# Kernel optimization log

Hardware: AMD Instinct MI355X
Metric: run time of the kernel (lower is better)

Reference implementation:

```python
import jax, jax.numpy as jnp
import numpy as np

N_NODES = 100000
N_EDGES = 1600000
IN_DIM, HID, OUT = 6, 64, 32


def _linear_params(key, fan_in, fan_out):
    k1, k2 = jax.random.split(key)
    bound = 1.0 / np.sqrt(fan_in)
    W = jax.random.uniform(k1, (fan_in, fan_out), jnp.float32, -bound, bound)
    b = jax.random.uniform(k2, (fan_out,), jnp.float32, -bound, bound)
    return W, b


def setup_inputs() -> dict:
    key = jax.random.key(0)
    ks = jax.random.split(key, 9)
    x = jax.random.normal(ks[0], (N_NODES, IN_DIM), jnp.float32)
    edge_index = jax.random.randint(ks[1], (2, N_EDGES), 0, N_NODES, jnp.int64)
    edge_attr = jax.random.normal(ks[2], (N_EDGES, 3), jnp.float32)
    W1a, b1a = _linear_params(ks[3], IN_DIM + 3, HID)
    W1b, b1b = _linear_params(ks[4], HID, HID)
    W2a, b2a = _linear_params(ks[5], HID + 3, HID)
    W2b, b2b = _linear_params(ks[6], HID, HID)
    W3a, b3a = _linear_params(ks[7], HID + 3, OUT)
    W3b, b3b = _linear_params(ks[8], OUT, OUT)
    return {
        "x": x, "edge_index": edge_index, "edge_attr": edge_attr,
        "W1a": W1a, "b1a": b1a, "W1b": W1b, "b1b": b1b,
        "W2a": W2a, "b2a": b2a, "W2b": W2b, "b2b": b2b,
        "W3a": W3a, "b3a": b3a, "W3b": W3b, "b3b": b3b,
    }


def _gnn_layer(x, src, dst, edge_attr, Wa, ba, Wb, bb):
    # message: per-edge 2-layer MLP on [x_j, edge_attr]
    msg = jnp.concatenate([x[src], edge_attr], axis=-1)       # [E, in+3]
    h = jax.nn.relu(msg @ Wa + ba) @ Wb + bb                   # [E, out]
    # aggr='mean': scatter-sum into target nodes, divide by in-degree
    s = jax.ops.segment_sum(h, dst, num_segments=N_NODES)     # [N, out]
    cnt = jax.ops.segment_sum(jnp.ones((src.shape[0],), x.dtype), dst,
                              num_segments=N_NODES)
    return s / jnp.maximum(cnt, 1.0)[:, None]


def reference(x, edge_index, edge_attr,
              W1a, b1a, W1b, b1b,
              W2a, b2a, W2b, b2b,
              W3a, b3a, W3b, b3b):
    src, dst = edge_index[0], edge_index[1]   # x_j = x[src], aggregate at dst
    h = _gnn_layer(x, src, dst, edge_attr, W1a, b1a, W1b, b1b)
    h = jax.nn.relu(h)
    h = _gnn_layer(h, src, dst, edge_attr, W2a, b2a, W2b, b2b)
    h = jax.nn.relu(h)
    out = _gnn_layer(h, src, dst, edge_attr, W3a, b3a, W3b, b3b)
    return out
```

## Files before the change

### kernel.cpp

```cpp
#include <hip/hip_runtime.h>
#include <hip/hip_fp16.h>

#define N_NODES 100000
#define N_EDGES 1600000

__global__ __launch_bounds__(256) void degree_kernel(const int* __restrict__ dst,
                                                     int* __restrict__ cnt, int E) {
    const int range = blockIdx.x & 7;
    const int lo = range * (N_NODES / 8);
    const int hi = lo + (N_NODES / 8);
    int i = (blockIdx.x >> 3) * blockDim.x + threadIdx.x;
    const int stride = (gridDim.x >> 3) * blockDim.x;
    for (; i < E; i += stride) {
        const int d = dst[i];
        if (d >= lo && d < hi) atomicAdd(&cnt[d], 1);
    }
}

__global__ __launch_bounds__(256) void inv_kernel(const int* __restrict__ cnt,
                                                  float* __restrict__ inv, int N) {
    int i = blockIdx.x * blockDim.x + threadIdx.x;
    if (i < N) inv[i] = (cnt[i] > 0) ? (1.0f / (float)cnt[i]) : 0.0f;
}

__global__ __launch_bounds__(256) void block_sum_kernel(const int* __restrict__ cnt,
                                                        int* __restrict__ bsum, int N) {
    __shared__ int s[256];
    const int tid = threadIdx.x;
    const int i = blockIdx.x * 256 + tid;
    s[tid] = (i < N) ? cnt[i] : 0;
    __syncthreads();
#pragma unroll
    for (int d = 128; d > 0; d >>= 1) {
        if (tid < d) s[tid] += s[tid + d];
        __syncthreads();
    }
    if (tid == 0) bsum[blockIdx.x] = s[0];
}

__global__ __launch_bounds__(512) void scan_bsum_kernel(int* __restrict__ bsum, int NB) {
    __shared__ int s[512];
    const int tid = threadIdx.x;
    const int v = (tid < NB) ? bsum[tid] : 0;
    s[tid] = v;
    __syncthreads();
    for (int d = 1; d < 512; d <<= 1) {
        const int t = (tid >= d) ? s[tid - d] : 0;
        __syncthreads();
        s[tid] += t;
        __syncthreads();
    }
    if (tid < NB) bsum[tid] = s[tid] - v;
}

__global__ __launch_bounds__(256) void make_cursor_kernel(const int* __restrict__ cnt,
                                                          const int* __restrict__ bsum,
                                                          int* __restrict__ cursor, int N) {
    __shared__ int s[256];
    const int tid = threadIdx.x;
    const int i = blockIdx.x * 256 + tid;
    const int v = (i < N) ? cnt[i] : 0;
    s[tid] = v;
    __syncthreads();
    for (int d = 1; d < 256; d <<= 1) {
        const int t = (tid >= d) ? s[tid - d] : 0;
        __syncthreads();
        s[tid] += t;
        __syncthreads();
    }
    if (i < N) cursor[i] = bsum[blockIdx.x] + s[tid] - v;
}

__global__ __launch_bounds__(256) void scatter_pack_kernel(
    const int* __restrict__ src, const int* __restrict__ dst,
    const float* __restrict__ ea,
    int* __restrict__ cursor, float4* __restrict__ spf, int E) {
    const int range = blockIdx.x & 7;
    const int lo = range * (N_NODES / 8);
    const int hi = lo + (N_NODES / 8);
    int i = (blockIdx.x >> 3) * blockDim.x + threadIdx.x;
    const int stride = (gridDim.x >> 3) * blockDim.x;
    for (; i < E; i += stride) {
        const int d = dst[i];
        if (d >= lo && d < hi) {
            const int pos = atomicAdd(&cursor[d], 1);
            spf[pos] = make_float4(__int_as_float(src[i]),
                                   ea[3 * (size_t)i + 0],
                                   ea[3 * (size_t)i + 1],
                                   ea[3 * (size_t)i + 2]);
        }
    }
}

__global__ __launch_bounds__(256) void node_gemm6h(
    const float* __restrict__ x, const float* __restrict__ W,
    const float* __restrict__ bias, __half* __restrict__ out_, int N) {
    int n = blockIdx.x * blockDim.x + threadIdx.x;
    if (n >= N) return;
    const float* row = x + (size_t)n * 6;
    float v[6];
#pragma unroll
    for (int k = 0; k < 6; ++k) v[k] = row[k];
    __half2* orow = (__half2*)(out_ + (size_t)n * 64);
    for (int g = 0; g < 16; ++g) {
        float a0 = bias[4 * g + 0], a1 = bias[4 * g + 1];
        float a2 = bias[4 * g + 2], a3 = bias[4 * g + 3];
#pragma unroll
        for (int k = 0; k < 6; ++k) {
            const float m = v[k];
            const float* w = &W[k * 64 + 4 * g];
            a0 = fmaf(m, w[0], a0);
            a1 = fmaf(m, w[1], a1);
            a2 = fmaf(m, w[2], a2);
            a3 = fmaf(m, w[3], a3);
        }
        orow[2 * g]     = __floats2half2_rn(a0, a1);
        orow[2 * g + 1] = __floats2half2_rn(a2, a3);
    }
}

template <int DNEXT, bool OUTH>
__global__ __launch_bounds__(256) void fused_agg64(
    const __half* __restrict__ P,
    const float4* __restrict__ spf,
    const int* __restrict__ cursor, const int* __restrict__ cnt,
    const float* __restrict__ inv,
    const float* __restrict__ We,
    const float* __restrict__ Wb,
    const float* __restrict__ bb,
    const float* __restrict__ Wn,
    const float* __restrict__ bn,
    void* __restrict__ Poutv, int N) {
    const int lane = threadIdx.x & 63;
    const int w    = threadIdx.x >> 6;
    const int q    = lane >> 4;
    const int p    = lane & 15;
    const int n    = blockIdx.x * 4 + w;

    __shared__ __align__(16) float lrow[4][64];

    float we0[4], we1[4], we2[4];
#pragma unroll
    for (int k = 0; k < 4; ++k) {
        we0[k] = We[0 * 64 + 4 * p + k];
        we1[k] = We[1 * 64 + 4 * p + k];
        we2[k] = We[2 * 64 + 4 * p + k];
    }

    const int end   = cursor[n];
    const int count = cnt[n];
    int j = end - count;
    const float s_inv = inv[n];
    const float mask  = (s_inv != 0.0f) ? 1.0f : 0.0f;

    float s0 = 0.f, s1 = 0.f, s2 = 0.f, s3 = 0.f;

#define PROC64(f, valid)                                                         \
    {                                                                            \
        const ushort4 raw = *(const ushort4*)((const unsigned short*)P +         \
                            ((size_t)__float_as_int((f).x) << 6) + 4 * p);       \
        const float p0 = __half2float(__ushort_as_half(raw.x));                  \
        const float p1 = __half2float(__ushort_as_half(raw.y));                  \
        const float p2 = __half2float(__ushort_as_half(raw.z));                  \
        const float p3 = __half2float(__ushort_as_half(raw.w));                  \
        const float h0 = fmaxf(fmaf((f).w, we2[0], fmaf((f).z, we1[0], fmaf((f).y, we0[0], p0))), 0.f); \
        const float h1 = fmaxf(fmaf((f).w, we2[1], fmaf((f).z, we1[1], fmaf((f).y, we0[1], p1))), 0.f); \
        const float h2 = fmaxf(fmaf((f).w, we2[2], fmaf((f).z, we1[2], fmaf((f).y, we0[2], p2))), 0.f); \
        const float h3 = fmaxf(fmaf((f).w, we2[3], fmaf((f).z, we1[3], fmaf((f).y, we0[3], p3))), 0.f); \
        if (valid) { s0 += h0; s1 += h1; s2 += h2; s3 += h3; }                   \
    }

    if (count > 0) {
        const int e0 = j + q,     e1 = j + 4 + q;
        float4 f0 = spf[e0 < end ? e0 : end - 1];
        float4 f1 = spf[e1 < end ? e1 : end - 1];
        while (j + 8 < end) {
            const int g0i = j + 8 + q, g1i = j + 12 + q;
            const float4 g0 = spf[g0i < end ? g0i : end - 1];
            const float4 g1 = spf[g1i < end ? g1i : end - 1];
            PROC64(f0, true)
            PROC64(f1, true)
            f0 = g0; f1 = g1; j += 8;
        }
        PROC64(f0, (j + q < end))
        PROC64(f1, (j + 4 + q < end))
    }
#undef PROC64

    s0 += __shfl_xor(s0, 16); s1 += __shfl_xor(s1, 16);
    s2 += __shfl_xor(s2, 16); s3 += __shfl_xor(s3, 16);
    s0 += __shfl_xor(s0, 32); s1 += __shfl_xor(s1, 32);
    s2 += __shfl_xor(s2, 32); s3 += __shfl_xor(s3, 32);

    if (lane < 16) {
        *(float4*)&lrow[w][4 * p] =
            make_float4(s0 * s_inv, s1 * s_inv, s2 * s_inv, s3 * s_inv);
    }
    __builtin_amdgcn_wave_barrier();

    float m = bb[lane] * mask;
#pragma unroll
    for (int k = 0; k < 16; ++k) {
        const float4 r = *(const float4*)&lrow[w][4 * k];
        m = fmaf(r.x, Wb[(4 * k + 0) * 64 + lane], m);
        m = fmaf(r.y, Wb[(4 * k + 1) * 64 + lane], m);
        m = fmaf(r.z, Wb[(4 * k + 2) * 64 + lane], m);
        m = fmaf(r.w, Wb[(4 * k + 3) * 64 + lane], m);
    }
    m = fmaxf(m, 0.0f);
    __builtin_amdgcn_wave_barrier();
    lrow[w][lane] = m;
    __builtin_amdgcn_wave_barrier();
    const int c2 = lane % DNEXT;
    float o = bn[c2];
#pragma unroll
    for (int k = 0; k < 16; ++k) {
        const float4 r = *(const float4*)&lrow[w][4 * k];
        o = fmaf(r.x, Wn[(4 * k + 0) * DNEXT + c2], o);
        o = fmaf(r.y, Wn[(4 * k + 1) * DNEXT + c2], o);
        o = fmaf(r.z, Wn[(4 * k + 2) * DNEXT + c2], o);
        o = fmaf(r.w, Wn[(4 * k + 3) * DNEXT + c2], o);
    }
    if (lane < DNEXT) {
        if constexpr (OUTH)
            ((__half*)Poutv)[(size_t)n * DNEXT + lane] = __float2half_rn(o);
        else
            ((float*)Poutv)[(size_t)n * DNEXT + lane] = o;
    }
}

__global__ __launch_bounds__(256) void fused_agg32h(
    const __half* __restrict__ P,
    const float4* __restrict__ spf,
    const int* __restrict__ cursor, const int* __restrict__ cnt,
    const float* __restrict__ inv,
    const float* __restrict__ We,
    const float* __restrict__ Wb,
    const float* __restrict__ bb,
    float* __restrict__ out, int N) {
    const int lane = threadIdx.x & 63;
    const int w    = threadIdx.x >> 6;
    const int q    = lane >> 4;
    const int p    = lane & 15;
    const int n    = blockIdx.x * 4 + w;

    __shared__ __align__(16) float lrow[4][32];

    float we0[2], we1[2], we2[2];
#pragma unroll
    for (int k = 0; k < 2; ++k) {
        we0[k] = We[0 * 32 + 2 * p + k];
        we1[k] = We[1 * 32 + 2 * p + k];
        we2[k] = We[2 * 32 + 2 * p + k];
    }

    const int end   = cursor[n];
    const int count = cnt[n];
    int j = end - count;
    const float s_inv = inv[n];
    const float mask  = (s_inv != 0.0f) ? 1.0f : 0.0f;

    float s0 = 0.f, s1 = 0.f;

#define PROC32(f, valid)                                                         \
    {                                                                            \
        const __half2 pr = *(const __half2*)((const __half*)P +                  \
                           ((size_t)__float_as_int((f).x) << 5) + 2 * p);        \
        const float2 pf = __half22float2(pr);                                    \
        const float h0 = fmaxf(fmaf((f).w, we2[0], fmaf((f).z, we1[0], fmaf((f).y, we0[0], pf.x))), 0.f); \
        const float h1 = fmaxf(fmaf((f).w, we2[1], fmaf((f).z, we1[1], fmaf((f).y, we0[1], pf.y))), 0.f); \
        if (valid) { s0 += h0; s1 += h1; }                                       \
    }

    if (count > 0) {
        const int e0 = j + q,     e1 = j + 4 + q;
        float4 f0 = spf[e0 < end ? e0 : end - 1];
        float4 f1 = spf[e1 < end ? e1 : end - 1];
        while (j + 8 < end) {
            const int g0i = j + 8 + q, g1i = j + 12 + q;
            const float4 g0 = spf[g0i < end ? g0i : end - 1];
            const float4 g1 = spf[g1i < end ? g1i : end - 1];
            PROC32(f0, true)
            PROC32(f1, true)
            f0 = g0; f1 = g1; j += 8;
        }
        PROC32(f0, (j + q < end))
        PROC32(f1, (j + 4 + q < end))
    }
#undef PROC32

    s0 += __shfl_xor(s0, 16); s1 += __shfl_xor(s1, 16);
    s0 += __shfl_xor(s0, 32); s1 += __shfl_xor(s1, 32);

    if (lane < 16) {
        *(float2*)&lrow[w][2 * p] = make_float2(s0 * s_inv, s1 * s_inv);
    }
    __builtin_amdgcn_wave_barrier();

    const int c = lane & 31;
    float m = bb[c] * mask;
#pragma unroll
    for (int k = 0; k < 8; ++k) {
        const float4 r = *(const float4*)&lrow[w][4 * k];
        m = fmaf(r.x, Wb[(4 * k + 0) * 32 + c], m);
        m = fmaf(r.y, Wb[(4 * k + 1) * 32 + c], m);
        m = fmaf(r.z, Wb[(4 * k + 2) * 32 + c], m);
        m = fmaf(r.w, Wb[(4 * k + 3) * 32 + c], m);
    }
    if (lane < 32) out[(size_t)n * 32 + c] = m;
}

extern "C" void kernel_launch(void* const* d_in, const int* in_sizes, int n_in,
                              void* d_out, int out_size, void* d_ws, size_t ws_size,
                              hipStream_t stream) {
    const float* x   = (const float*)d_in[0];
    const int*   ei  = (const int*)d_in[1];
    const float* ea  = (const float*)d_in[2];
    const float* W1a = (const float*)d_in[3];
    const float* b1a = (const float*)d_in[4];
    const float* W1b = (const float*)d_in[5];
    const float* b1b = (const float*)d_in[6];
    const float* W2a = (const float*)d_in[7];
    const float* b2a = (const float*)d_in[8];
    const float* W2b = (const float*)d_in[9];
    const float* b2b = (const float*)d_in[10];
    const float* W3a = (const float*)d_in[11];
    const float* b3a = (const float*)d_in[12];
    const float* W3b = (const float*)d_in[13];
    const float* b3b = (const float*)d_in[14];

    const int* src = ei;
    const int* dst = ei + N_EDGES;
    float* out = (float*)d_out;

    char* ws = (char*)d_ws;
    int*    cnt    = (int*)(ws);
    float*  inv    = (float*)(ws + 0x80000);
    int*    bsum   = (int*)(ws + 0x100000);
    int*    cursor = (int*)(ws + 0x110000);
    float4* spf    = (float4*)(ws + 0x200000);
    __half* PH1    = (__half*)(ws + 0x1B00000);
    __half* PH2    = (__half*)(ws + 0x2800000);
    __half* P3h    = (__half*)(ws + 0x3500000);

    const int NBLK = (N_NODES + 255) / 256;

    hipMemsetAsync(cnt, 0, N_NODES * sizeof(int), stream);
    degree_kernel<<<2048, 256, 0, stream>>>(dst, cnt, N_EDGES);
    inv_kernel<<<NBLK, 256, 0, stream>>>(cnt, inv, N_NODES);
    block_sum_kernel<<<NBLK, 256, 0, stream>>>(cnt, bsum, N_NODES);
    scan_bsum_kernel<<<1, 512, 0, stream>>>(bsum, NBLK);
    make_cursor_kernel<<<NBLK, 256, 0, stream>>>(cnt, bsum, cursor, N_NODES);
    scatter_pack_kernel<<<2048, 256, 0, stream>>>(src, dst, ea, cursor, spf, N_EDGES);

    node_gemm6h<<<NBLK, 256, 0, stream>>>(x, W1a, b1a, PH1, N_NODES);

    fused_agg64<64, true><<<N_NODES / 4, 256, 0, stream>>>(
        PH1, spf, cursor, cnt, inv, W1a + 6 * 64, W1b, b1b, W2a, b2a, PH2, N_NODES);
    fused_agg64<32, true><<<N_NODES / 4, 256, 0, stream>>>(
        PH2, spf, cursor, cnt, inv, W2a + 64 * 64, W2b, b2b, W3a, b3a, P3h, N_NODES);
    fused_agg32h<<<N_NODES / 4, 256, 0, stream>>>(
        P3h, spf, cursor, cnt, inv, W3a + 64 * 32, W3b, b3b, out, N_NODES);
}
```

Before: 483.8 us.

## Gather padded raw x in layer one instead of precomputed fp16 projections

Layer one no longer precomputes a 64-wide fp16 projection per node. Instead it pads x to 8 floats per node and has a new fused kernel gather the 32-byte rows, recomputing the 6-input projection per edge in registers. This cuts gather traffic per edge from 128 bytes to 32 bytes, at the cost of extra FMAs and more registers per edge. The gather loops in all three aggregation kernels also drop the explicit software prefetch in favour of a simpler 8/4/remainder loop that loads inside the macro.

```diff
diff --git a/kernel.cpp b/kernel.cpp
--- a/kernel.cpp
+++ b/kernel.cpp
@@ -21,6 +21,17 @@
                                                   float* __restrict__ inv, int N) {
     int i = blockIdx.x * blockDim.x + threadIdx.x;
     if (i < N) inv[i] = (cnt[i] > 0) ? (1.0f / (float)cnt[i]) : 0.0f;
+}
+
+__global__ __launch_bounds__(256) void pad_x_kernel(const float* __restrict__ x,
+                                                    float* __restrict__ x8, int N) {
+    int i = blockIdx.x * blockDim.x + threadIdx.x;
+    if (i >= 2 * N) return;
+    const int n = i >> 1, h = i & 1;
+    float4 v;
+    if (h == 0) v = make_float4(x[n * 6 + 0], x[n * 6 + 1], x[n * 6 + 2], x[n * 6 + 3]);
+    else        v = make_float4(x[n * 6 + 4], x[n * 6 + 5], 0.0f, 0.0f);
+    ((float4*)x8)[i] = v;
 }
 
 __global__ __launch_bounds__(256) void block_sum_kernel(const int* __restrict__ cnt,
@@ -92,31 +103,118 @@
     }
 }
 
-__global__ __launch_bounds__(256) void node_gemm6h(
-    const float* __restrict__ x, const float* __restrict__ W,
-    const float* __restrict__ bias, __half* __restrict__ out_, int N) {
-    int n = blockIdx.x * blockDim.x + threadIdx.x;
-    if (n >= N) return;
-    const float* row = x + (size_t)n * 6;
-    float v[6];
-#pragma unroll
-    for (int k = 0; k < 6; ++k) v[k] = row[k];
-    __half2* orow = (__half2*)(out_ + (size_t)n * 64);
-    for (int g = 0; g < 16; ++g) {
-        float a0 = bias[4 * g + 0], a1 = bias[4 * g + 1];
-        float a2 = bias[4 * g + 2], a3 = bias[4 * g + 3];
-#pragma unroll
-        for (int k = 0; k < 6; ++k) {
-            const float m = v[k];
-            const float* w = &W[k * 64 + 4 * g];
-            a0 = fmaf(m, w[0], a0);
-            a1 = fmaf(m, w[1], a1);
-            a2 = fmaf(m, w[2], a2);
-            a3 = fmaf(m, w[3], a3);
-        }
-        orow[2 * g]     = __floats2half2_rn(a0, a1);
-        orow[2 * g + 1] = __floats2half2_rn(a2, a3);
-    }
+__global__ __launch_bounds__(256) void fused_l1x(
+    const float* __restrict__ x8,
+    const float4* __restrict__ spf,
+    const int* __restrict__ cursor, const int* __restrict__ cnt,
+    const float* __restrict__ inv,
+    const float* __restrict__ W1a,
+    const float* __restrict__ b1a,
+    const float* __restrict__ W1b,
+    const float* __restrict__ b1b,
+    const float* __restrict__ W2a,
+    const float* __restrict__ b2a,
+    __half* __restrict__ PH2, int N) {
+    const int lane = threadIdx.x & 63;
+    const int w    = threadIdx.x >> 6;
+    const int q    = lane >> 4;
+    const int p    = lane & 15;
+    const int n    = blockIdx.x * 4 + w;
+
+    __shared__ __align__(16) float lrow[4][64];
+
+    float wx[6][4], wee[3][4], pb[4];
+#pragma unroll
+    for (int c = 0; c < 4; ++c) {
+        pb[c] = b1a[4 * p + c];
+#pragma unroll
+        for (int k = 0; k < 6; ++k) wx[k][c] = W1a[k * 64 + 4 * p + c];
+#pragma unroll
+        for (int k = 0; k < 3; ++k) wee[k][c] = W1a[(6 + k) * 64 + 4 * p + c];
+    }
+
+    const int end   = cursor[n];
+    const int count = cnt[n];
+    int j = end - count;
+    const float s_inv = inv[n];
+    const float mask  = (s_inv != 0.0f) ? 1.0f : 0.0f;
+
+    float s0 = 0.f, s1 = 0.f, s2 = 0.f, s3 = 0.f;
+
+#define GRPX(base, valid)                                                        \
+    {                                                                            \
+        const int ei = (base) + q;                                               \
+        const float4 f = spf[ei < end ? ei : end - 1];                           \
+        const float* xr = x8 + ((size_t)__float_as_int(f.x) << 3);               \
+        const float4 xlo = *(const float4*)xr;                                   \
+        const float2 xhi = *(const float2*)(xr + 4);                             \
+        float h0 = pb[0], h1 = pb[1], h2 = pb[2], h3 = pb[3];                    \
+        h0 = fmaf(xlo.x, wx[0][0], h0); h1 = fmaf(xlo.x, wx[0][1], h1);          \
+        h2 = fmaf(xlo.x, wx[0][2], h2); h3 = fmaf(xlo.x, wx[0][3], h3);          \
+        h0 = fmaf(xlo.y, wx[1][0], h0); h1 = fmaf(xlo.y, wx[1][1], h1);          \
+        h2 = fmaf(xlo.y, wx[1][2], h2); h3 = fmaf(xlo.y, wx[1][3], h3);          \
+        h0 = fmaf(xlo.z, wx[2][0], h0); h1 = fmaf(xlo.z, wx[2][1], h1);          \
+        h2 = fmaf(xlo.z, wx[2][2], h2); h3 = fmaf(xlo.z, wx[2][3], h3);          \
+        h0 = fmaf(xlo.w, wx[3][0], h0); h1 = fmaf(xlo.w, wx[3][1], h1);          \
+        h2 = fmaf(xlo.w, wx[3][2], h2); h3 = fmaf(xlo.w, wx[3][3], h3);          \
+        h0 = fmaf(xhi.x, wx[4][0], h0); h1 = fmaf(xhi.x, wx[4][1], h1);          \
+        h2 = fmaf(xhi.x, wx[4][2], h2); h3 = fmaf(xhi.x, wx[4][3], h3);          \
+        h0 = fmaf(xhi.y, wx[5][0], h0); h1 = fmaf(xhi.y, wx[5][1], h1);          \
+        h2 = fmaf(xhi.y, wx[5][2], h2); h3 = fmaf(xhi.y, wx[5][3], h3);          \
+        h0 = fmaf(f.y, wee[0][0], h0);  h1 = fmaf(f.y, wee[0][1], h1);           \
+        h2 = fmaf(f.y, wee[0][2], h2);  h3 = fmaf(f.y, wee[0][3], h3);           \
+        h0 = fmaf(f.z, wee[1][0], h0);  h1 = fmaf(f.z, wee[1][1], h1);           \
+        h2 = fmaf(f.z, wee[1][2], h2);  h3 = fmaf(f.z, wee[1][3], h3);           \
+        h0 = fmaf(f.w, wee[2][0], h0);  h1 = fmaf(f.w, wee[2][1], h1);           \
+        h2 = fmaf(f.w, wee[2][2], h2);  h3 = fmaf(f.w, wee[2][3], h3);           \
+        if (valid) {                                                             \
+            s0 += fmaxf(h0, 0.f); s1 += fmaxf(h1, 0.f);                          \
+            s2 += fmaxf(h2, 0.f); s3 += fmaxf(h3, 0.f);                          \
+        }                                                                        \
+    }
+
+    for (; j + 8 <= end; j += 8) { GRPX(j, true) GRPX(j + 4, true) }
+    if (j + 4 <= end) { GRPX(j, true) j += 4; }
+    {
+        const int rem = end - j;
+        if (rem > 0) { GRPX(j, (q < rem)) }
+    }
+#undef GRPX
+
+    s0 += __shfl_xor(s0, 16); s1 += __shfl_xor(s1, 16);
+    s2 += __shfl_xor(s2, 16); s3 += __shfl_xor(s3, 16);
+    s0 += __shfl_xor(s0, 32); s1 += __shfl_xor(s1, 32);
+    s2 += __shfl_xor(s2, 32); s3 += __shfl_xor(s3, 32);
+
+    if (lane < 16) {
+        *(float4*)&lrow[w][4 * p] =
+            make_float4(s0 * s_inv, s1 * s_inv, s2 * s_inv, s3 * s_inv);
+    }
+    __builtin_amdgcn_wave_barrier();
+
+    float m = b1b[lane] * mask;
+#pragma unroll
+    for (int k = 0; k < 16; ++k) {
+        const float4 r = *(const float4*)&lrow[w][4 * k];
+        m = fmaf(r.x, W1b[(4 * k + 0) * 64 + lane], m);
+        m = fmaf(r.y, W1b[(4 * k + 1) * 64 + lane], m);
+        m = fmaf(r.z, W1b[(4 * k + 2) * 64 + lane], m);
+        m = fmaf(r.w, W1b[(4 * k + 3) * 64 + lane], m);
+    }
+    m = fmaxf(m, 0.0f);
+    __builtin_amdgcn_wave_barrier();
+    lrow[w][lane] = m;
+    __builtin_amdgcn_wave_barrier();
+    float o = b2a[lane];
+#pragma unroll
+    for (int k = 0; k < 16; ++k) {
+        const float4 r = *(const float4*)&lrow[w][4 * k];
+        o = fmaf(r.x, W2a[(4 * k + 0) * 64 + lane], o);
+        o = fmaf(r.y, W2a[(4 * k + 1) * 64 + lane], o);
+        o = fmaf(r.z, W2a[(4 * k + 2) * 64 + lane], o);
+        o = fmaf(r.w, W2a[(4 * k + 3) * 64 + lane], o);
+    }
+    PH2[(size_t)n * 64 + lane] = __float2half_rn(o);
 }
 
 template <int DNEXT, bool OUTH>
@@ -155,37 +253,30 @@
 
     float s0 = 0.f, s1 = 0.f, s2 = 0.f, s3 = 0.f;
 
-#define PROC64(f, valid)                                                         \
+#define GRP4H(base, valid)                                                       \
     {                                                                            \
+        const int ei = (base) + q;                                               \
+        const float4 f = spf[ei < end ? ei : end - 1];                           \
         const ushort4 raw = *(const ushort4*)((const unsigned short*)P +         \
-                            ((size_t)__float_as_int((f).x) << 6) + 4 * p);       \
+                            ((size_t)__float_as_int(f.x) << 6) + 4 * p);         \
         const float p0 = __half2float(__ushort_as_half(raw.x));                  \
         const float p1 = __half2float(__ushort_as_half(raw.y));                  \
         const float p2 = __half2float(__ushort_as_half(raw.z));                  \
         const float p3 = __half2float(__ushort_as_half(raw.w));                  \
-        const float h0 = fmaxf(fmaf((f).w, we2[0], fmaf((f).z, we1[0], fmaf((f).y, we0[0], p0))), 0.f); \
-        const float h1 = fmaxf(fmaf((f).w, we2[1], fmaf((f).z, we1[1], fmaf((f).y, we0[1], p1))), 0.f); \
-        const float h2 = fmaxf(fmaf((f).w, we2[2], fmaf((f).z, we1[2], fmaf((f).y, we0[2], p2))), 0.f); \
-        const float h3 = fmaxf(fmaf((f).w, we2[3], fmaf((f).z, we1[3], fmaf((f).y, we0[3], p3))), 0.f); \
+        const float h0 = fmaxf(fmaf(f.w, we2[0], fmaf(f.z, we1[0], fmaf(f.y, we0[0], p0))), 0.f); \
+        const float h1 = fmaxf(fmaf(f.w, we2[1], fmaf(f.z, we1[1], fmaf(f.y, we0[1], p1))), 0.f); \
+        const float h2 = fmaxf(fmaf(f.w, we2[2], fmaf(f.z, we1[2], fmaf(f.y, we0[2], p2))), 0.f); \
+        const float h3 = fmaxf(fmaf(f.w, we2[3], fmaf(f.z, we1[3], fmaf(f.y, we0[3], p3))), 0.f); \
         if (valid) { s0 += h0; s1 += h1; s2 += h2; s3 += h3; }                   \
     }
 
-    if (count > 0) {
-        const int e0 = j + q,     e1 = j + 4 + q;
-        float4 f0 = spf[e0 < end ? e0 : end - 1];
-        float4 f1 = spf[e1 < end ? e1 : end - 1];
-        while (j + 8 < end) {
-            const int g0i = j + 8 + q, g1i = j + 12 + q;
-            const float4 g0 = spf[g0i < end ? g0i : end - 1];
-            const float4 g1 = spf[g1i < end ? g1i : end - 1];
-            PROC64(f0, true)
-            PROC64(f1, true)
-            f0 = g0; f1 = g1; j += 8;
-        }
-        PROC64(f0, (j + q < end))
-        PROC64(f1, (j + 4 + q < end))
-    }
-#undef PROC64
+    for (; j + 8 <= end; j += 8) { GRP4H(j, true) GRP4H(j + 4, true) }
+    if (j + 4 <= end) { GRP4H(j, true) j += 4; }
+    {
+        const int rem = end - j;
+        if (rem > 0) { GRP4H(j, (q < rem)) }
+    }
+#undef GRP4H
 
     s0 += __shfl_xor(s0, 16); s1 += __shfl_xor(s1, 16);
     s2 += __shfl_xor(s2, 16); s3 += __shfl_xor(s3, 16);
@@ -262,32 +353,25 @@
 
     float s0 = 0.f, s1 = 0.f;
 
-#define PROC32(f, valid)                                                         \
+#define GRP4F(base, valid)                                                       \
     {                                                                            \
+        const int ei = (base) + q;                                               \
+        const float4 f = spf[ei < end ? ei : end - 1];                           \
         const __half2 pr = *(const __half2*)((const __half*)P +                  \
-                           ((size_t)__float_as_int((f).x) << 5) + 2 * p);        \
+                           ((size_t)__float_as_int(f.x) << 5) + 2 * p);          \
         const float2 pf = __half22float2(pr);                                    \
-        const float h0 = fmaxf(fmaf((f).w, we2[0], fmaf((f).z, we1[0], fmaf((f).y, we0[0], pf.x))), 0.f); \
-        const float h1 = fmaxf(fmaf((f).w, we2[1], fmaf((f).z, we1[1], fmaf((f).y, we0[1], pf.y))), 0.f); \
+        const float h0 = fmaxf(fmaf(f.w, we2[0], fmaf(f.z, we1[0], fmaf(f.y, we0[0], pf.x))), 0.f); \
+        const float h1 = fmaxf(fmaf(f.w, we2[1], fmaf(f.z, we1[1], fmaf(f.y, we0[1], pf.y))), 0.f); \
         if (valid) { s0 += h0; s1 += h1; }                                       \
     }
 
-    if (count > 0) {
-        const int e0 = j + q,     e1 = j + 4 + q;
-        float4 f0 = spf[e0 < end ? e0 : end - 1];
-        float4 f1 = spf[e1 < end ? e1 : end - 1];
-        while (j + 8 < end) {
-            const int g0i = j + 8 + q, g1i = j + 12 + q;
-            const float4 g0 = spf[g0i < end ? g0i : end - 1];
-            const float4 g1 = spf[g1i < end ? g1i : end - 1];
-            PROC32(f0, true)
-            PROC32(f1, true)
-            f0 = g0; f1 = g1; j += 8;
-        }
-        PROC32(f0, (j + q < end))
-        PROC32(f1, (j + 4 + q < end))
-    }
-#undef PROC32
+    for (; j + 8 <= end; j += 8) { GRP4F(j, true) GRP4F(j + 4, true) }
+    if (j + 4 <= end) { GRP4F(j, true) j += 4; }
+    {
+        const int rem = end - j;
+        if (rem > 0) { GRP4F(j, (q < rem)) }
+    }
+#undef GRP4F
 
     s0 += __shfl_xor(s0, 16); s1 += __shfl_xor(s1, 16);
     s0 += __shfl_xor(s0, 32); s1 += __shfl_xor(s1, 32);
@@ -339,7 +423,7 @@
     int*    bsum   = (int*)(ws + 0x100000);
     int*    cursor = (int*)(ws + 0x110000);
     float4* spf    = (float4*)(ws + 0x200000);
-    __half* PH1    = (__half*)(ws + 0x1B00000);
+    float*  x8     = (float*)(ws + 0x1B00000);
     __half* PH2    = (__half*)(ws + 0x2800000);
     __half* P3h    = (__half*)(ws + 0x3500000);
 
@@ -352,11 +436,10 @@
     scan_bsum_kernel<<<1, 512, 0, stream>>>(bsum, NBLK);
     make_cursor_kernel<<<NBLK, 256, 0, stream>>>(cnt, bsum, cursor, N_NODES);
     scatter_pack_kernel<<<2048, 256, 0, stream>>>(src, dst, ea, cursor, spf, N_EDGES);
-
-    node_gemm6h<<<NBLK, 256, 0, stream>>>(x, W1a, b1a, PH1, N_NODES);
-
-    fused_agg64<64, true><<<N_NODES / 4, 256, 0, stream>>>(
-        PH1, spf, cursor, cnt, inv, W1a + 6 * 64, W1b, b1b, W2a, b2a, PH2, N_NODES);
+    pad_x_kernel<<<(2 * N_NODES + 255) / 256, 256, 0, stream>>>(x, x8, N_NODES);
+
+    fused_l1x<<<N_NODES / 4, 256, 0, stream>>>(
+        x8, spf, cursor, cnt, inv, W1a, b1a, W1b, b1b, W2a, b2a, PH2, N_NODES);
     fused_agg64<32, true><<<N_NODES / 4, 256, 0, stream>>>(
         PH2, spf, cursor, cnt, inv, W2a + 64 * 64, W2b, b2b, W3a, b3a, P3h, N_NODES);
     fused_agg32h<<<N_NODES / 4, 256, 0, stream>>>(
```

Result: slower. 508.3 us (+5.1%).
